# Performance work log

Hardware: AMD Instinct MI355X
Metric: run time of the kernel (lower is better)

Reference implementation:

```python
import jax, jax.numpy as jnp
import numpy as np

IN_F = 4096
OUT_F = 11008
GROUP = 128
BATCH = 32
Q_OUT = OUT_F // 2          # two int4 values packed per byte along out dim
N_GROUPS = IN_F // GROUP    # 32 groups


def setup_inputs() -> dict:
    key = jax.random.key(0)
    k1, k2, k3, k4, k5 = jax.random.split(key, 5)
    inp = jax.random.normal(k1, (BATCH, 1, IN_F), dtype=jnp.float32)
    qweight = jax.random.randint(k2, (IN_F, Q_OUT), 0, 256, dtype=jnp.int32)   # packed bytes
    scales = jax.random.uniform(k3, (N_GROUPS, OUT_F), dtype=jnp.float32) * 0.01
    qzeros = jax.random.randint(k4, (N_GROUPS, Q_OUT), 0, 256, dtype=jnp.int32)  # packed bytes
    bias = jax.random.normal(k5, (OUT_F,), dtype=jnp.float32)
    return {"input": inp, "qweight": qweight, "scales": scales, "qzeros": qzeros, "bias": bias}


def _unpack_int4(packed, n_out):
    # packed: [rows, n_out//2] bytes; low nibble -> even out col, high nibble -> odd out col
    low = packed & 0xF
    high = (packed >> 4) & 0xF
    return jnp.stack([low, high], axis=-1).reshape(packed.shape[0], n_out)


def reference(input, qweight, scales, qzeros, bias):
    # GPTQ-style grouped dequant: w[k, n] = (q[k, n] - zero[g(k), n]) * scale[g(k), n]
    q = _unpack_int4(qweight, OUT_F).astype(jnp.float32)   # [K, N]
    z = _unpack_int4(qzeros, OUT_F).astype(jnp.float32)    # [G, N]
    gidx = jnp.arange(IN_F) // GROUP                       # [K] group index per input channel
    w = (q - z[gidx]) * scales[gidx]                       # [K, N] dequantized weight
    # decode GEMV/GEMM: [B, 1, K] x [K, N] -> [B, 1, N], plus bias (mm_bias_int4 path)
    return jnp.einsum('bsk,kn->bsn', input, w) + bias
```

## Files before the change

### kernel.cpp

```cpp
#include <hip/hip_runtime.h>
#include <cstdint>

#define IN_F 4096
#define OUT_F 11008
#define Q_OUT 5504
#define GROUP 128
#define BATCH 32

#define KBS 8
#define GPB 4
#define NCH 8
#define BN 64
#define BST 18

typedef int   i32x4 __attribute__((ext_vector_type(4)));
typedef float f32x4 __attribute__((ext_vector_type(4)));

__global__ __launch_bounds__(256)
void prep_kernel(const float* __restrict__ x,
                 const float* __restrict__ bias,
                 uint4* __restrict__ xq,
                 int*   __restrict__ Sx,
                 float* __restrict__ delta,
                 float* __restrict__ out)
{
    const int t = threadIdx.x;
    if (blockIdx.x >= 32) {
        const int j4 = ((blockIdx.x - 32) * 256 + t) * 4;
        *reinterpret_cast<float4*>(out + j4) =
            *reinterpret_cast<const float4*>(bias + (j4 % OUT_F));
        return;
    }
    const int m = blockIdx.x;
    const float* xr = x + (size_t)m * IN_F + t * 16;
    float4 v[4];
    #pragma unroll
    for (int i = 0; i < 4; ++i) v[i] = reinterpret_cast<const float4*>(xr)[i];

    float lm = 0.f;
    #pragma unroll
    for (int i = 0; i < 4; ++i) {
        lm = fmaxf(lm, fmaxf(fmaxf(fabsf(v[i].x), fabsf(v[i].y)),
                             fmaxf(fabsf(v[i].z), fabsf(v[i].w))));
    }
    #pragma unroll
    for (int d = 32; d; d >>= 1) lm = fmaxf(lm, __shfl_xor(lm, d));
    __shared__ float wred[4];
    if ((t & 63) == 0) wred[t >> 6] = lm;
    __syncthreads();
    const float mx  = fmaxf(fmaxf(wred[0], wred[1]), fmaxf(wred[2], wred[3]));
    const float inv = mx > 0.f ? 127.0f / mx : 0.f;

    int q[16];
    #pragma unroll
    for (int i = 0; i < 4; ++i) {
        q[i * 4 + 0] = __float2int_rn(v[i].x * inv);
        q[i * 4 + 1] = __float2int_rn(v[i].y * inv);
        q[i * 4 + 2] = __float2int_rn(v[i].z * inv);
        q[i * 4 + 3] = __float2int_rn(v[i].w * inv);
    }
    uint4 w;
    uint* wp = reinterpret_cast<uint*>(&w);
    #pragma unroll
    for (int i = 0; i < 4; ++i)
        wp[i] = (q[i*4] & 255) | ((q[i*4+1] & 255) << 8) |
                ((q[i*4+2] & 255) << 16) | ((q[i*4+3] & 255) << 24);
    xq[(t >> 2) * 128 + (m >> 4) * 64 + (t & 3) * 16 + (m & 15)] = w;

    int psum = 0;
    #pragma unroll
    for (int i = 0; i < 16; ++i) psum += q[i];
    #pragma unroll
    for (int d = 4; d; d >>= 1) psum += __shfl_down(psum, d, 8);
    if ((t & 7) == 0) Sx[(t >> 3) * 32 + m] = psum;
    if (t == 0) delta[m] = mx * (1.0f / 127.0f);
}

__global__ __launch_bounds__(256, 4)
void int4_gemm_i8(const uint4* __restrict__ xq,
                  const int*   __restrict__ qw,
                  const float* __restrict__ scales,
                  const int*   __restrict__ qz,
                  const int*   __restrict__ Sx,
                  const float* __restrict__ delta,
                  float*       __restrict__ out)
{
    const int tid  = threadIdx.x;
    const int lane = tid & 63;
    const int wid  = tid >> 6;
    const int nb   = blockIdx.x;
    const int kb   = blockIdx.y;
    const int g0   = kb * GPB;
    const int k0b  = g0 * GROUP;

    __shared__ uint4 a_lds[1024];
    __shared__ int   b_lds[2][64 * BST];

    const int cl  = lane & 15;
    const int kg  = lane >> 4;
    const int n   = nb * BN + wid * 16 + cl;
    const int shn = (cl & 1) * 4;

    #pragma unroll
    for (int r = 0; r < 4; ++r) {
        const uint4* gp = xq + (size_t)kb * 1024 + r * 256 + tid;
        __builtin_amdgcn_global_load_lds(
            (const __attribute__((address_space(1))) uint32_t*)gp,
            (__attribute__((address_space(3))) uint32_t*)&a_lds[r * 256 + wid * 64],
            16, 0, 0);
    }

    int   zv[GPB];
    float sv[GPB];
    #pragma unroll
    for (int g = 0; g < GPB; ++g) {
        sv[g] = scales[(size_t)(g0 + g) * OUT_F + n];
        zv[g] = (qz[(size_t)(g0 + g) * Q_OUT + (n >> 1)] >> shn) & 15;
    }

    const int a16 = tid & 15;
    const int rk  = tid >> 4;

    uint2 d[2][4];
    i32x4 acc_i[2] = {};
    f32x4 accf[2]  = {};
    int4  sx0v = {}, sx1v = {};

    auto LOADB = [&](int c, int set) {
        const int kr = k0b + c * 64 + 4 * rk;
        #pragma unroll
        for (int i = 0; i < 4; ++i)
            d[set][i] = *reinterpret_cast<const uint2*>(
                qw + (size_t)(kr + i) * Q_OUT + nb * 32 + 2 * a16);
    };
    auto WLDS = [&](int buf, int set) {
        #pragma unroll
        for (int j = 0; j < 2; ++j) {
            uint b0 = (j ? d[set][0].y : d[set][0].x) & 255u;
            uint b1 = (j ? d[set][1].y : d[set][1].x) & 255u;
            uint b2 = (j ? d[set][2].y : d[set][2].x) & 255u;
            uint b3 = (j ? d[set][3].y : d[set][3].x) & 255u;
            uint p  = b0 | (b1 << 8) | (b2 << 16) | (b3 << 24);
            const int nloc = 4 * a16 + 2 * j;
            b_lds[buf][(nloc + 0) * BST + rk] = (int)(p & 0x0F0F0F0Fu);
            b_lds[buf][(nloc + 1) * BST + rk] = (int)((p >> 4) & 0x0F0F0F0Fu);
        }
    };

    LOADB(0, 0);
    LOADB(1, 1);
    WLDS(0, 0);
    asm volatile("s_waitcnt vmcnt(0) lgkmcnt(0)" ::: "memory");
    __builtin_amdgcn_s_barrier();
    asm volatile("" ::: "memory");

    #pragma unroll
    for (int c = 0; c < NCH; ++c) {
        const int cur = c & 1;
        const int gl  = c >> 1;
        if (c + 2 < NCH) LOADB(c + 2, cur);
        if ((c & 1) == 0) {
            sx0v = *reinterpret_cast<const int4*>(Sx + (g0 + gl) * 32 + kg * 4);
            sx1v = *reinterpret_cast<const int4*>(Sx + (g0 + gl) * 32 + 16 + kg * 4);
        }

        const int* bp = &b_lds[cur][(wid * 16 + cl) * BST + 4 * kg];
        int2 qa = *reinterpret_cast<const int2*>(bp);
        int2 qb = *reinterpret_cast<const int2*>(bp + 2);
        i32x4 bv; bv[0] = qa.x; bv[1] = qa.y; bv[2] = qb.x; bv[3] = qb.y;

        uint4 a0 = a_lds[(c * 2 + 0) * 64 + lane];
        uint4 a1 = a_lds[(c * 2 + 1) * 64 + lane];
        acc_i[0] = __builtin_amdgcn_mfma_i32_16x16x64_i8(
            __builtin_bit_cast(i32x4, a0), bv, acc_i[0], 0, 0, 0);
        acc_i[1] = __builtin_amdgcn_mfma_i32_16x16x64_i8(
            __builtin_bit_cast(i32x4, a1), bv, acc_i[1], 0, 0, 0);

        if (c & 1) {
            const int   zz = zv[gl];
            const float ss = sv[gl];
            int sxa[8] = { sx0v.x, sx0v.y, sx0v.z, sx0v.w,
                           sx1v.x, sx1v.y, sx1v.z, sx1v.w };
            #pragma unroll
            for (int f = 0; f < 2; ++f)
                #pragma unroll
                for (int r = 0; r < 4; ++r) {
                    int tt = acc_i[f][r] - zz * sxa[f * 4 + r];
                    accf[f][r] = fmaf(ss, (float)tt, accf[f][r]);
                }
            acc_i[0] = i32x4{0, 0, 0, 0};
            acc_i[1] = i32x4{0, 0, 0, 0};
        }

        if (c + 1 < NCH) {
            WLDS(cur ^ 1, cur ^ 1);
            asm volatile("s_waitcnt lgkmcnt(0)" ::: "memory");
            __builtin_amdgcn_s_barrier();
            asm volatile("" ::: "memory");
        }
    }

    float4 dl0 = *reinterpret_cast<const float4*>(delta + kg * 4);
    float4 dl1 = *reinterpret_cast<const float4*>(delta + 16 + kg * 4);
    const float dla[8] = { dl0.x, dl0.y, dl0.z, dl0.w, dl1.x, dl1.y, dl1.z, dl1.w };
    #pragma unroll
    for (int f = 0; f < 2; ++f)
        #pragma unroll
        for (int r = 0; r < 4; ++r) {
            const int m = f * 16 + kg * 4 + r;
            unsafeAtomicAdd(out + (size_t)m * OUT_F + n, dla[f * 4 + r] * accf[f][r]);
        }
}

extern "C" void kernel_launch(void* const* d_in, const int* in_sizes, int n_in,
                              void* d_out, int out_size, void* d_ws, size_t ws_size,
                              hipStream_t stream)
{
    const float* inp    = (const float*)d_in[0];
    const int*   qw     = (const int*)d_in[1];
    const float* scales = (const float*)d_in[2];
    const int*   qz     = (const int*)d_in[3];
    const float* bias   = (const float*)d_in[4];
    float*       out    = (float*)d_out;

    uint4* xq    = (uint4*)d_ws;
    int*   Sx    = (int*)((char*)d_ws + 131072);
    float* delta = (float*)((char*)d_ws + 131072 + 4096);

    prep_kernel<<<376, 256, 0, stream>>>(inp, bias, xq, Sx, delta, out);

    int4_gemm_i8<<<dim3(OUT_F / BN, KBS), 256, 0, stream>>>(
        xq, qw, scales, qz, Sx, delta, out);
}
```

Before: 28.41 us.

## Halve K-split, stream activations via registers, store packed nibbles in LDS

The K split drops from 8 to 4 blocks, so each block handles 8 groups across 16 chunks, which halves the atomic-add traffic into the output. The activation tile no longer goes through LDS: each wave double-buffers its A fragments from global memory straight into registers. Weight bytes are now written to LDS still packed, and each lane unpacks its own nibble at read time with a shift and mask, which halves LDS stores and footprint. The bias-initialisation blocks also write four float4s per thread, and the launch-bounds occupancy hint drops to 3, allowing more registers per thread at the cost of fewer resident blocks and fewer blocks in the grid overall.

```diff
diff --git a/kernel.cpp b/kernel.cpp
--- a/kernel.cpp
+++ b/kernel.cpp
@@ -7,9 +7,9 @@
 #define GROUP 128
 #define BATCH 32
 
-#define KBS 8
-#define GPB 4
-#define NCH 8
+#define KBS 4
+#define GPB 8
+#define NCH 16
 #define BN 64
 #define BST 18
 
@@ -26,9 +26,11 @@
 {
     const int t = threadIdx.x;
     if (blockIdx.x >= 32) {
-        const int j4 = ((blockIdx.x - 32) * 256 + t) * 4;
-        *reinterpret_cast<float4*>(out + j4) =
-            *reinterpret_cast<const float4*>(bias + (j4 % OUT_F));
+        const int base = (blockIdx.x - 32) * 4096 + t * 16;
+        #pragma unroll
+        for (int i = 0; i < 4; ++i)
+            *reinterpret_cast<float4*>(out + base + i * 4) =
+                *reinterpret_cast<const float4*>(bias + ((base + i * 4) % OUT_F));
         return;
     }
     const int m = blockIdx.x;
@@ -76,7 +78,7 @@
     if (t == 0) delta[m] = mx * (1.0f / 127.0f);
 }
 
-__global__ __launch_bounds__(256, 4)
+__global__ __launch_bounds__(256, 3)
 void int4_gemm_i8(const uint4* __restrict__ xq,
                   const int*   __restrict__ qw,
                   const float* __restrict__ scales,
@@ -93,22 +95,13 @@
     const int g0   = kb * GPB;
     const int k0b  = g0 * GROUP;
 
-    __shared__ uint4 a_lds[1024];
-    __shared__ int   b_lds[2][64 * BST];
+    __shared__ int b_lds[2][32 * BST];
 
     const int cl  = lane & 15;
     const int kg  = lane >> 4;
     const int n   = nb * BN + wid * 16 + cl;
+    const int w   = wid * 8 + (cl >> 1);
     const int shn = (cl & 1) * 4;
-
-    #pragma unroll
-    for (int r = 0; r < 4; ++r) {
-        const uint4* gp = xq + (size_t)kb * 1024 + r * 256 + tid;
-        __builtin_amdgcn_global_load_lds(
-            (const __attribute__((address_space(1))) uint32_t*)gp,
-            (__attribute__((address_space(3))) uint32_t*)&a_lds[r * 256 + wid * 64],
-            16, 0, 0);
-    }
 
     int   zv[GPB];
     float sv[GPB];
@@ -122,6 +115,7 @@
     const int rk  = tid >> 4;
 
     uint2 d[2][4];
+    uint4 A[2][2];
     i32x4 acc_i[2] = {};
     f32x4 accf[2]  = {};
     int4  sx0v = {}, sx1v = {};
@@ -132,6 +126,11 @@
         for (int i = 0; i < 4; ++i)
             d[set][i] = *reinterpret_cast<const uint2*>(
                 qw + (size_t)(kr + i) * Q_OUT + nb * 32 + 2 * a16);
+    };
+    auto LOADA = [&](int c, int set) {
+        const uint4* ab = xq + (size_t)kb * (NCH * 128) + c * 128;
+        A[set][0] = ab[lane];
+        A[set][1] = ab[64 + lane];
     };
     auto WLDS = [&](int buf, int set) {
         #pragma unroll
@@ -140,17 +139,17 @@
             uint b1 = (j ? d[set][1].y : d[set][1].x) & 255u;
             uint b2 = (j ? d[set][2].y : d[set][2].x) & 255u;
             uint b3 = (j ? d[set][3].y : d[set][3].x) & 255u;
-            uint p  = b0 | (b1 << 8) | (b2 << 16) | (b3 << 24);
-            const int nloc = 4 * a16 + 2 * j;
-            b_lds[buf][(nloc + 0) * BST + rk] = (int)(p & 0x0F0F0F0Fu);
-            b_lds[buf][(nloc + 1) * BST + rk] = (int)((p >> 4) & 0x0F0F0F0Fu);
+            b_lds[buf][(2 * a16 + j) * BST + rk] =
+                (int)(b0 | (b1 << 8) | (b2 << 16) | (b3 << 24));
         }
     };
 
     LOADB(0, 0);
+    LOADA(0, 0);
     LOADB(1, 1);
+    LOADA(1, 1);
     WLDS(0, 0);
-    asm volatile("s_waitcnt vmcnt(0) lgkmcnt(0)" ::: "memory");
+    asm volatile("s_waitcnt lgkmcnt(0)" ::: "memory");
     __builtin_amdgcn_s_barrier();
     asm volatile("" ::: "memory");
 
@@ -164,17 +163,20 @@
             sx1v = *reinterpret_cast<const int4*>(Sx + (g0 + gl) * 32 + 16 + kg * 4);
         }
 
-        const int* bp = &b_lds[cur][(wid * 16 + cl) * BST + 4 * kg];
-        int2 qa = *reinterpret_cast<const int2*>(bp);
-        int2 qb = *reinterpret_cast<const int2*>(bp + 2);
-        i32x4 bv; bv[0] = qa.x; bv[1] = qa.y; bv[2] = qb.x; bv[3] = qb.y;
-
-        uint4 a0 = a_lds[(c * 2 + 0) * 64 + lane];
-        uint4 a1 = a_lds[(c * 2 + 1) * 64 + lane];
+        const int* bp = &b_lds[cur][w * BST + 4 * kg];
+        int4 qp = *reinterpret_cast<const int4*>(bp);
+        i32x4 bv;
+        bv[0] = (int)(((uint)qp.x >> shn) & 0x0F0F0F0Fu);
+        bv[1] = (int)(((uint)qp.y >> shn) & 0x0F0F0F0Fu);
+        bv[2] = (int)(((uint)qp.z >> shn) & 0x0F0F0F0Fu);
+        bv[3] = (int)(((uint)qp.w >> shn) & 0x0F0F0F0Fu);
+
         acc_i[0] = __builtin_amdgcn_mfma_i32_16x16x64_i8(
-            __builtin_bit_cast(i32x4, a0), bv, acc_i[0], 0, 0, 0);
+            __builtin_bit_cast(i32x4, A[cur][0]), bv, acc_i[0], 0, 0, 0);
         acc_i[1] = __builtin_amdgcn_mfma_i32_16x16x64_i8(
-            __builtin_bit_cast(i32x4, a1), bv, acc_i[1], 0, 0, 0);
+            __builtin_bit_cast(i32x4, A[cur][1]), bv, acc_i[1], 0, 0, 0);
+
+        if (c + 2 < NCH) LOADA(c + 2, cur);
 
         if (c & 1) {
             const int   zz = zv[gl];
@@ -227,7 +229,7 @@
     int*   Sx    = (int*)((char*)d_ws + 131072);
     float* delta = (float*)((char*)d_ws + 131072 + 4096);
 
-    prep_kernel<<<376, 256, 0, stream>>>(inp, bias, xq, Sx, delta, out);
+    prep_kernel<<<118, 256, 0, stream>>>(inp, bias, xq, Sx, delta, out);
 
     int4_gemm_i8<<<dim3(OUT_F / BN, KBS), 256, 0, stream>>>(
         xq, qw, scales, qz, Sx, delta, out);
```

After: 30.39 us. 1.07x slower.
